# Kernel optimization log

Hardware: AMD Instinct MI355X
Metric: run time of the kernel (lower is better)

## Reference

```python
import jax, jax.numpy as jnp
import numpy as np

ITERS = 4
LN_EPS = 1e-5


def build_grid(H, W):
    # standard uORF grid in [-1, 1], shape (H, W, 2), last dim = (x, y)
    x = jnp.linspace(-1.0 + 1.0 / W, 1.0 - 1.0 / W, W)
    y = jnp.linspace(-1.0 + 1.0 / H, 1.0 - 1.0 / H, H)
    yy, xx = jnp.meshgrid(y, x, indexing='ij')
    return jnp.stack([xx, yy], axis=-1)


def ln(x, g, b):
    m = jnp.mean(x, axis=-1, keepdims=True)
    v = jnp.var(x, axis=-1, keepdims=True)
    return (x - m) * jax.lax.rsqrt(v + LN_EPS) * g + b


def setup_inputs():
    key = jax.random.key(0)
    ks = jax.random.split(key, 16)
    B, H, W, C, K, Ds = 4, 64, 64, 256, 5, 256
    s = 0.02
    inp = {
        'feat': jax.random.normal(ks[0], (B, H, W, C), jnp.float32),
        'mask': (jax.random.uniform(ks[1], (K, 1, H, W)) > 0.5).astype(jnp.float32),
        'noise': jax.random.normal(ks[2], (B, K, Ds), jnp.float32),
        'slots_mu': jax.random.normal(ks[3], (1, 1, Ds), jnp.float32),
        'slots_logsigma': jax.random.normal(ks[4], (1, 1, Ds), jnp.float32) * s,
        'norm_g': jnp.ones((C,), jnp.float32), 'norm_b': jnp.zeros((C,), jnp.float32),
        'grid_W': jax.random.normal(ks[5], (C, 4), jnp.float32) * s,
        'grid_b': jnp.zeros((C,), jnp.float32),
        'k_W': jax.random.normal(ks[6], (C, C), jnp.float32) * s,
        'v_W': jax.random.normal(ks[7], (C, C), jnp.float32) * s,
        'mlp_g': jnp.ones((C,), jnp.float32), 'mlp_b': jnp.zeros((C,), jnp.float32),
        'mlp_W': jax.random.normal(ks[8], (Ds, C), jnp.float32) * s,
        'mlp_bias': jnp.zeros((Ds,), jnp.float32),
        'q_g': jnp.ones((Ds,), jnp.float32), 'q_b': jnp.zeros((Ds,), jnp.float32),
        'q_W': jax.random.normal(ks[9], (Ds, Ds), jnp.float32) * s,
        'gru_Wih': jax.random.normal(ks[10], (3 * Ds, Ds), jnp.float32) * s,
        'gru_Whh': jax.random.normal(ks[11], (3 * Ds, Ds), jnp.float32) * s,
        'gru_bih': jnp.zeros((3 * Ds,), jnp.float32),
        'gru_bhh': jnp.zeros((3 * Ds,), jnp.float32),
        'res_g': jnp.ones((Ds,), jnp.float32), 'res_b': jnp.zeros((Ds,), jnp.float32),
        'res_W': jax.random.normal(ks[12], (Ds, Ds), jnp.float32) * s,
        'res_bias': jnp.zeros((Ds,), jnp.float32),
    }
    return inp


def reference(feat, mask, noise, slots_mu, slots_logsigma, norm_g, norm_b,
              grid_W, grid_b, k_W, v_W, mlp_g, mlp_b, mlp_W, mlp_bias,
              q_g, q_b, q_W, gru_Wih, gru_Whh, gru_bih, gru_bhh,
              res_g, res_b, res_W, res_bias):
    B, H, W, C = feat.shape
    K = mask.shape[0]
    N = H * W
    Ds = slots_mu.shape[-1]
    scale = Ds ** -0.5

    grid = build_grid(H, W)                                   # (H, W, 2)
    # foreground positions: mask-weighted mean of grid -> (K, 2)
    g = jnp.transpose(grid, (2, 0, 1))[None]                  # (1, 2, H, W)
    fg_pos = jnp.sum(g * mask, axis=(2, 3)) / (jnp.sum(mask, axis=(2, 3)) + 1e-5)
    fg_pos = jnp.broadcast_to(fg_pos[None], (B, K, 2))        # (B, K, 2)

    feat_n = ln(feat.reshape(B, N, C), norm_g, norm_b)        # (B, N, C)
    mask_flat = mask.reshape(K, N)
    slot = slots_mu + jnp.exp(slots_logsigma) * noise         # (B, K, Ds)

    # k, v with relative position embedding; fg_pos never changes in-loop,
    # so compute once (the original recomputes the same values each iter).
    rel = grid.reshape(1, 1, N, 2) - fg_pos[:, :, None, :]    # (B, K, N, 2)
    rel4 = jnp.concatenate([rel, -rel], axis=-1)              # (B, K, N, 4)
    ge = rel4 @ grid_W.T + grid_b                             # (B, K, N, C)
    kbase = feat_n @ k_W.T                                    # (B, N, C)
    vbase = feat_n @ v_W.T
    kk = ln(kbase[:, None] + ge, mlp_g, mlp_b) @ mlp_W.T + mlp_bias  # (B,K,N,Ds)
    vv = ln(vbase[:, None] + ge, mlp_g, mlp_b) @ mlp_W.T + mlp_bias

    attn_vis = None
    for _ in range(ITERS):
        slot_prev = slot
        q = ln(slot, q_g, q_b) @ q_W.T                        # (B, K, Ds)
        attn = jnp.einsum('bkd,bknd->bkn', q, kk) * scale
        attn = jnp.where(mask_flat[None] == 0, -1e9, attn)
        attn = jax.nn.softmax(attn, axis=-1)                  # (B, K, N)
        upd = jnp.einsum('bkn,bknd->bkd', attn, vv)           # (B, K, Ds)
        # torch GRUCell
        x = upd.reshape(-1, Ds)
        h = slot.reshape(-1, Ds)
        gi = x @ gru_Wih.T + gru_bih
        gh = h @ gru_Whh.T + gru_bhh
        ir, iz, inn = jnp.split(gi, 3, axis=-1)
        hr, hz, hn = jnp.split(gh, 3, axis=-1)
        r = jax.nn.sigmoid(ir + hr)
        z = jax.nn.sigmoid(iz + hz)
        n = jnp.tanh(inn + r * hn)
        hnew = ((1.0 - z) * n + z * h).reshape(B, K, Ds)
        slot = (ln(hnew, res_g, res_b) @ res_W.T + res_bias) + slot_prev
        amin = attn.min(axis=-1, keepdims=True)
        amax = attn.max(axis=-1, keepdims=True)
        attn_vis = (attn - amin) / (amax - amin + 1e-5)
    return slot, fg_pos, attn_vis
```

## Files before the change

kernel.cpp:

```cpp
#include <hip/hip_runtime.h>
#include <math.h>

typedef unsigned short u16;
typedef unsigned int   u32;
typedef short bf8v __attribute__((ext_vector_type(8)));
typedef float f4v  __attribute__((ext_vector_type(4)));

static constexpr int B_=4, C_=256, K_=5, D_=256, N_=4096, IT_=4;
static constexpr int LP_=264;
static constexpr int PREP_N=2839;
static constexpr float EPS_=1e-5f;

__device__ __forceinline__ float bf2f(u16 u){ u32 x=((u32)u)<<16; float f; __builtin_memcpy(&f,&x,4); return f; }
__device__ __forceinline__ float bflo(u32 u){ u32 x=u<<16; float f; __builtin_memcpy(&f,&x,4); return f; }
__device__ __forceinline__ float bfhi(u32 u){ u32 x=u&0xffff0000u; float f; __builtin_memcpy(&f,&x,4); return f; }
__device__ __forceinline__ u16 f2bf(float f){ u32 x; __builtin_memcpy(&x,&f,4); u32 r=x+0x7fffu+((x>>16)&1u); return (u16)(r>>16); }
__device__ __forceinline__ float ldin(const void* p, size_t i, int f){
  return f ? ((const float*)p)[i] : bf2f(((const u16*)p)[i]);
}
__device__ __forceinline__ void stout(void* p, size_t i, float v, int f){
  if (f) ((float*)p)[i]=v; else ((u16*)p)[i]=f2bf(v);
}

__device__ __forceinline__ void breduce4(float&a,float&b,float&c,float&d,float* red){
  #pragma unroll
  for(int o=32;o>0;o>>=1){
    a+=__shfl_down(a,o,64); b+=__shfl_down(b,o,64);
    c+=__shfl_down(c,o,64); d+=__shfl_down(d,o,64);
  }
  int w=threadIdx.x>>6;
  __syncthreads();
  if((threadIdx.x&63)==0){ red[w]=a; red[4+w]=b; red[8+w]=c; red[12+w]=d; }
  __syncthreads();
  a=red[0]+red[1]+red[2]+red[3];
  b=red[4]+red[5]+red[6]+red[7];
  c=red[8]+red[9]+red[10]+red[11];
  d=red[12]+red[13]+red[14]+red[15];
}
__device__ __forceinline__ void breduce4_16(float&a,float&b,float&c,float&d,float* red){
  #pragma unroll
  for(int o=32;o>0;o>>=1){
    a+=__shfl_down(a,o,64); b+=__shfl_down(b,o,64);
    c+=__shfl_down(c,o,64); d+=__shfl_down(d,o,64);
  }
  int w=threadIdx.x>>6;
  __syncthreads();
  if((threadIdx.x&63)==0){ red[w]=a; red[16+w]=b; red[32+w]=c; red[48+w]=d; }
  __syncthreads();
  a=0;b=0;c=0;d=0;
  #pragma unroll
  for(int i=0;i<16;++i){ a+=red[i]; b+=red[16+i]; c+=red[32+i]; d+=red[48+i]; }
}

__global__ void probe_kernel(const void* feat, int* flag){
  __shared__ float red[16];
  const u32* p=(const u32*)feat;
  int t=threadIdx.x; int bad=0;
  for(int s=0;s<8;++s){
    u32 wd=p[t+s*256];
    float lo=bf2f((u16)(wd&0xffffu));
    if(!(fabsf(lo)<1e6f)) bad++;
  }
  float bb=(float)bad, z1=0,z2=0,z3=0;
  breduce4(bb,z1,z2,z3,red);
  if(t==0) *flag = (bb>=16.f)?1:0;
}

__global__ void prep1_kernel(const int* flag,
    const void* kW, const void* vW, const void* mW, const void* qW, const void* rW,
    const void* Wih, const void* Whh, const void* mu, const void* lsig, const void* noise,
    const void* gW, const void* gb_, const void* mg,
    const void* mb_, const void* mbias, const void* mask,
    float* WqT, float* WrT, float* WihT, float* WhhT,
    float* slot, float* gvec,
    u16* Wkb, u16* Wvb, u16* Wgb,
    float* Uvec, float* Qs, float* fg, void* out)
{
  int f=*flag;
  int bid=blockIdx.x;
  int t=threadIdx.x;
  if(bid<PREP_N){
    int e=bid*256+t;
    if(e<65536){ int c=e>>8, r=e&255; WqT[e]=ldin(qW,(size_t)r*256+c,f); return;} e-=65536;
    if(e<65536){ int c=e>>8, r=e&255; WrT[e]=ldin(rW,(size_t)r*256+c,f); return;} e-=65536;
    if(e<196608){ int c=e/768, r=e-c*768; WihT[e]=ldin(Wih,(size_t)r*256+c,f); return;} e-=196608;
    if(e<196608){ int c=e/768, r=e-c*768; WhhT[e]=ldin(Whh,(size_t)r*256+c,f); return;} e-=196608;
    if(e<5120){ int d=e&255; slot[e]=ldin(mu,d,f)+expf(ldin(lsig,d,f))*ldin(noise,e,f); return;} e-=5120;
    if(e<768){
      int c=e&255, sel=e>>8;
      float v;
      if(sel==0)      v=ldin(gW,c*4+0,f)-ldin(gW,c*4+2,f);
      else if(sel==1) v=ldin(gW,c*4+1,f)-ldin(gW,c*4+3,f);
      else            v=ldin(gb_,c,f);
      gvec[e]=v; return;
    } e-=768;
    if(e<65536){ Wkb[e]=f2bf(ldin(kW,e,f)); return;} e-=65536;
    if(e<65536){ Wvb[e]=f2bf(ldin(vW,e,f)); return;} e-=65536;
    if(e<65536){ int c=e&255; Wgb[e]=f2bf(ldin(mg,c,f)*ldin(mW,e,f)); }
    return;
  }
  __shared__ float s_a[256], s_b[256], s_c[256], red[16];
  if(bid==PREP_N){
    s_a[t]=ldin(gW,t*4+0,f)-ldin(gW,t*4+2,f);
    s_b[t]=ldin(gW,t*4+1,f)-ldin(gW,t*4+3,f);
    s_c[t]=ldin(gb_,t,f);
    __syncthreads();
    float u1=0,u2=0,u3=0,gw=0,bw=0;
    #pragma unroll 8
    for(int c=0;c<256;++c){
      float mwv=ldin(mW,(size_t)t*256+c,f);
      float wg=ldin(mg,c,f)*mwv;
      u1+=s_a[c]*wg; u2+=s_b[c]*wg; u3+=s_c[c]*wg; gw+=wg;
      bw+=ldin(mb_,c,f)*mwv;
    }
    Uvec[t]=u1; Uvec[256+t]=u2; Uvec[512+t]=u3; Uvec[768+t]=gw;
    Uvec[1024+t]=bw+ldin(mbias,t,f);
    float a=s_a[t], b=s_b[t], cc=s_c[t];
    float s0=a*a,s1=b*b,s2=cc*cc,s3=a*b; breduce4(s0,s1,s2,s3,red);
    float s4=a*cc,s5=b*cc,s6=a,s7=b;     breduce4(s4,s5,s6,s7,red);
    float s8=cc,z1=0,z2=0,z3=0;          breduce4(s8,z1,z2,z3,red);
    if(t==0){
      Qs[0]=s0; Qs[1]=s1; Qs[2]=s2; Qs[3]=s3; Qs[4]=s4; Qs[5]=s5;
      Qs[6]=s6*(1.f/256.f); Qs[7]=s7*(1.f/256.f); Qs[8]=s8*(1.f/256.f);
    }
  } else {
    int k=bid-PREP_N-1;
    float sx=0,sy=0,sm=0;
    for(int s=0;s<16;++s){
      int p=t+s*256;
      float m=ldin(mask,(size_t)k*N_+p,f);
      int i=p>>6, j=p&63;
      float x=(2*j+1)*(1.0f/64.0f)-1.0f;
      float y=(2*i+1)*(1.0f/64.0f)-1.0f;
      sx+=x*m; sy+=y*m; sm+=m;
    }
    float d=0;
    breduce4(sx,sy,sm,d,red);
    if(t==0){
      float inv=1.0f/(sm+1e-5f);
      float fx=sx*inv, fy=sy*inv;
      fg[k*2]=fx; fg[k*2+1]=fy;
      for(int b=0;b<B_;++b){
        stout(out, 5120+(b*K_+k)*2+0, fx, f);
        stout(out, 5120+(b*K_+k)*2+1, fy, f);
      }
    }
  }
}

__global__ void __launch_bounds__(256) base_kernel(const int* flag, const void* feat, const void* ng, const void* nb,
    const u16* Wkb, const u16* Wvb, const u16* Wgb, const float* gvec,
    float* scal, u16* PkT, u16* Pvb,
    const float* slot, const void* qg, const void* qb_, const float* WqT, const float* Uvec,
    float* qbuf, float* qsc)
{
  __shared__ u16 fnb[16*LP_];
  __shared__ u16 kbL[16*LP_];
  __shared__ u16 vbL[16*LP_];
  int t=threadIdx.x, f=*flag;
  if(blockIdx.x>=1024){
    float* Lq=(float*)fnb; float* qsh=(float*)kbL; float* red=(float*)vbL;
    int bk=blockIdx.x-1024;
    float x=slot[bk*256+t];
    float s=x,s2=x*x,z0=0,z1=0; breduce4(s,s2,z0,z1,red);
    float m=s*(1.f/256.f), v=s2*(1.f/256.f)-m*m;
    Lq[t]=(x-m)*rsqrtf(v+EPS_)*ldin(qg,t,f)+ldin(qb_,t,f);
    __syncthreads();
    float acc=0;
    #pragma unroll 8
    for(int c=0;c<256;++c) acc+=Lq[c]*WqT[c*256+t];
    qbuf[bk*256+t]=acc; qsh[t]=acc;
    __syncthreads();
    float q=qsh[t];
    float s0=q*Uvec[t], s1=q*Uvec[256+t], s2b=q*Uvec[512+t], s3=q*Uvec[768+t];
    breduce4(s0,s1,s2b,s3,red);
    float s4=q*Uvec[1024+t], z2=0,z3=0,z4=0;
    breduce4(s4,z2,z3,z4,red);
    if(t==0){ qsc[bk*8+0]=s0; qsc[bk*8+1]=s1; qsc[bk*8+2]=s2b; qsc[bk*8+3]=s3; qsc[bk*8+4]=s4; }
    return;
  }
  int w=t>>6, l=t&63;
  int quad=l>>4, m=l&15;
  int row0=blockIdx.x*16;
  {
    float g0=ldin(ng,l,f), g1=ldin(ng,l+64,f), g2=ldin(ng,l+128,f), g3=ldin(ng,l+192,f);
    float b0=ldin(nb,l,f), b1=ldin(nb,l+64,f), b2=ldin(nb,l+128,f), b3=ldin(nb,l+192,f);
    #pragma unroll
    for(int r4=0;r4<4;++r4){
      int r=4*w+r4; size_t base=(size_t)(row0+r)*256;
      float x0=ldin(feat,base+l,f), x1=ldin(feat,base+l+64,f),
            x2=ldin(feat,base+l+128,f), x3=ldin(feat,base+l+192,f);
      float s=x0+x1+x2+x3, s2=x0*x0+x1*x1+x2*x2+x3*x3;
      #pragma unroll
      for(int o=32;o>0;o>>=1){ s+=__shfl_xor(s,o,64); s2+=__shfl_xor(s2,o,64); }
      float mm=s*(1.f/256.f), inv=rsqrtf(s2*(1.f/256.f)-mm*mm+EPS_);
      fnb[r*LP_+l]    =f2bf((x0-mm)*inv*g0+b0);
      fnb[r*LP_+l+64] =f2bf((x1-mm)*inv*g1+b1);
      fnb[r*LP_+l+128]=f2bf((x2-mm)*inv*g2+b2);
      fnb[r*LP_+l+192]=f2bf((x3-mm)*inv*g3+b3);
    }
  }
  __syncthreads();
  {
    f4v ack[4], acv[4];
    #pragma unroll
    for(int i=0;i<4;++i){ ack[i]=(f4v){0.f,0.f,0.f,0.f}; acv[i]=(f4v){0.f,0.f,0.f,0.f}; }
    #pragma unroll
    for(int kk=0;kk<8;++kk){
      int kb0=kk*32+quad*8;
      bf8v af=*(bf8v*)&fnb[m*LP_+kb0];
      #pragma unroll
      for(int i=0;i<4;++i){
        int n=64*w+16*i+m;
        bf8v bk=*(const bf8v*)(Wkb+(size_t)n*256+kb0);
        bf8v bv=*(const bf8v*)(Wvb+(size_t)n*256+kb0);
        ack[i]=__builtin_amdgcn_mfma_f32_16x16x32_bf16(af,bk,ack[i],0,0,0);
        acv[i]=__builtin_amdgcn_mfma_f32_16x16x32_bf16(af,bv,acv[i],0,0,0);
      }
    }
    #pragma unroll
    for(int i=0;i<4;++i){
      int n=64*w+16*i+m;
      #pragma unroll
      for(int r=0;r<4;++r){
        int row=quad*4+r;
        kbL[row*LP_+n]=f2bf(ack[i][r]);
        vbL[row*LP_+n]=f2bf(acv[i][r]);
      }
    }
  }
  __syncthreads();
  {
    float gA0=gvec[l], gA1=gvec[l+64], gA2=gvec[l+128], gA3=gvec[l+192];
    float gB0=gvec[256+l], gB1=gvec[256+l+64], gB2=gvec[256+l+128], gB3=gvec[256+l+192];
    float gC0=gvec[512+l], gC1=gvec[512+l+64], gC2=gvec[512+l+128], gC3=gvec[512+l+192];
    for(int r4=0;r4<4;++r4){
      int r=4*w+r4;
      float k0=bf2f(kbL[r*LP_+l]), k1=bf2f(kbL[r*LP_+l+64]),
            k2=bf2f(kbL[r*LP_+l+128]), k3=bf2f(kbL[r*LP_+l+192]);
      float x0=bf2f(vbL[r*LP_+l]), x1=bf2f(vbL[r*LP_+l+64]),
            x2=bf2f(vbL[r*LP_+l+128]), x3=bf2f(vbL[r*LP_+l+192]);
      float v0=k0+k1+k2+k3;
      float v1=k0*k0+k1*k1+k2*k2+k3*k3;
      float v2=k0*gA0+k1*gA1+k2*gA2+k3*gA3;
      float v3=k0*gB0+k1*gB1+k2*gB2+k3*gB3;
      float v4=k0*gC0+k1*gC1+k2*gC2+k3*gC3;
      float v5=x0+x1+x2+x3;
      float v6=x0*x0+x1*x1+x2*x2+x3*x3;
      float v7=x0*gA0+x1*gA1+x2*gA2+x3*gA3;
      float v8=x0*gB0+x1*gB1+x2*gB2+x3*gB3;
      float v9=x0*gC0+x1*gC1+x2*gC2+x3*gC3;
      #pragma unroll
      for(int o=32;o>0;o>>=1){
        v0+=__shfl_down(v0,o,64); v1+=__shfl_down(v1,o,64); v2+=__shfl_down(v2,o,64);
        v3+=__shfl_down(v3,o,64); v4+=__shfl_down(v4,o,64); v5+=__shfl_down(v5,o,64);
        v6+=__shfl_down(v6,o,64); v7+=__shfl_down(v7,o,64); v8+=__shfl_down(v8,o,64);
        v9+=__shfl_down(v9,o,64);
      }
      if(l==0){
        float* sc=scal+(size_t)(row0+r)*10;
        sc[0]=v0; sc[1]=v1; sc[2]=v2; sc[3]=v3; sc[4]=v4;
        sc[5]=v5; sc[6]=v6; sc[7]=v7; sc[8]=v8; sc[9]=v9;
      }
    }
  }
  {
    f4v apk[4], apv[4];
    #pragma unroll
    for(int i=0;i<4;++i){ apk[i]=(f4v){0.f,0.f,0.f,0.f}; apv[i]=(f4v){0.f,0.f,0.f,0.f}; }
    #pragma unroll
    for(int kk=0;kk<8;++kk){
      int kb0=kk*32+quad*8;
      bf8v afk=*(bf8v*)&kbL[m*LP_+kb0];
      bf8v afv=*(bf8v*)&vbL[m*LP_+kb0];
      #pragma unroll
      for(int i=0;i<4;++i){
        int n=64*w+16*i+m;
        bf8v bg=*(const bf8v*)(Wgb+(size_t)n*256+kb0);
        apk[i]=__builtin_amdgcn_mfma_f32_16x16x32_bf16(afk,bg,apk[i],0,0,0);
        apv[i]=__builtin_amdgcn_mfma_f32_16x16x32_bf16(afv,bg,apv[i],0,0,0);
      }
    }
    #pragma unroll
    for(int i=0;i<4;++i){
      int d=64*w+16*i+m;
      *(ushort4*)(PkT+(size_t)d*16384+row0+quad*4)=
        make_ushort4(f2bf(apk[i][0]),f2bf(apk[i][1]),f2bf(apk[i][2]),f2bf(apk[i][3]));
      #pragma unroll
      for(int r=0;r<4;++r)
        fnb[(quad*4+r)*LP_+d]=f2bf(apv[i][r]);
    }
  }
  __syncthreads();
  {
    int d0=l*4;
    #pragma unroll
    for(int r=0;r<4;++r){
      int row=4*w+r;
      ushort4 s4=make_ushort4(fnb[row*LP_+d0],fnb[row*LP_+d0+1],fnb[row*LP_+d0+2],fnb[row*LP_+d0+3]);
      *(ushort4*)(Pvb+(size_t)(row0+row)*256+d0)=s4;
    }
  }
}

__global__ void __launch_bounds__(512) attn_kernel(const int* flag, const float* qbuf, const u16* PkT,
    const float* scal, const float* Qs, const float* qsc, const float* fg, const void* mask,
    const u16* Pvb, float* logits, float* pmax, float* psum, float* updpart, float* sscp,
    int store_lg)
{
  __shared__ float q5[1280];
  __shared__ float un[10240];
  __shared__ float lgs[320], ivs[320], mvs[320];
  __shared__ float qs5[40], fgs[10], Qss[9], MSl[5];
  __shared__ float sred[8][5][4];
  int tid=threadIdx.x, f=*flag;
  int b=blockIdx.x>>6, ch=blockIdx.x&63;
  int w=tid>>6, l=tid&63;
  int n0=ch<<6;
  for(int p=tid;p<1280;p+=512) q5[p]=qbuf[(size_t)b*1280+p];
  if(tid<40) qs5[tid]=qsc[(size_t)b*40+tid];
  if(tid<10) fgs[tid]=fg[tid];
  if(tid<9)  Qss[tid]=Qs[tid];
  __syncthreads();
  {
    int n=n0+l; size_t row=(size_t)b*N_+n;
    float dk0=0,dk1=0,dk2=0,dk3=0,dk4=0;
    int cbase=w*32;
    #pragma unroll 8
    for(int cc=0;cc<32;++cc){
      int c=cbase+cc;
      float pv=bf2f(PkT[(size_t)c*16384+row]);
      dk0+=pv*q5[c]; dk1+=pv*q5[256+c]; dk2+=pv*q5[512+c];
      dk3+=pv*q5[768+c]; dk4+=pv*q5[1024+c];
    }
    un[(w*5+0)*64+l]=dk0; un[(w*5+1)*64+l]=dk1; un[(w*5+2)*64+l]=dk2;
    un[(w*5+3)*64+l]=dk3; un[(w*5+4)*64+l]=dk4;
  }
  __syncthreads();
  if(tid<320){
    int k=tid>>6, nl=tid&63;
    float dot=0;
    #pragma unroll
    for(int j=0;j<8;++j) dot+=un[(j*5+k)*64+nl];
    int n2=n0+nl; size_t row2=(size_t)b*N_+n2;
    const float* sc=scal+row2*10;
    float rx=(2*(n2&63)+1)*(1.f/64.f)-1.f-fgs[2*k];
    float ry=(2*(n2>>6)+1)*(1.f/64.f)-1.f-fgs[2*k+1];
    float qge=rx*rx*Qss[0]+ry*ry*Qss[1]+Qss[2]+2.f*(rx*ry*Qss[3]+rx*Qss[4]+ry*Qss[5]);
    float mk=sc[0]*(1.f/256.f)+rx*Qss[6]+ry*Qss[7]+Qss[8];
    float sxk=sc[1]+2.f*(rx*sc[2]+ry*sc[3]+sc[4])+qge;
    float invK=rsqrtf(sxk*(1.f/256.f)-mk*mk+EPS_);
    float lg=invK*(dot+rx*qs5[k*8+0]+ry*qs5[k*8+1]+qs5[k*8+2]-mk*qs5[k*8+3])+qs5[k*8+4];
    float mval=ldin(mask,(size_t)k*N_+n2,f);
    lg=(mval==0.f)? -1e9f : lg*0.0625f;
    if(store_lg) logits[((size_t)(b*5+k))*N_+n2]=lg;
    lgs[tid]=lg;
    float mv=sc[5]*(1.f/256.f)+rx*Qss[6]+ry*Qss[7]+Qss[8];
    float sxv=sc[6]+2.f*(rx*sc[7]+ry*sc[8]+sc[9])+qge;
    mvs[tid]=mv;
    ivs[tid]=rsqrtf(sxv*(1.f/256.f)-mv*mv+EPS_);
  }
  __syncthreads();
  if(tid<64){
    #pragma unroll
    for(int k=0;k<5;++k){
      float v=lgs[k*64+tid];
      float M=v;
      #pragma unroll
      for(int o=32;o>0;o>>=1) M=fmaxf(M,__shfl_xor(M,o,64));
      float e=expf(v-M);
      #pragma unroll
      for(int o=32;o>0;o>>=1) e+=__shfl_xor(e,o,64);
      if(tid==0){ pmax[((size_t)(b*64+ch))*5+k]=M; psum[((size_t)(b*64+ch))*5+k]=e; MSl[k]=M; }
    }
  }
  __syncthreads();
  {
    float acc[5][4]={{0}};
    float swx[5]={0,0,0,0,0}, swy[5]={0,0,0,0,0}, sw[5]={0,0,0,0,0}, swm[5]={0,0,0,0,0};
    #pragma unroll 2
    for(int rr=0;rr<8;++rr){
      int nl=w*8+rr; int n2=n0+nl;
      size_t row=(size_t)b*N_+n2;
      uint2 pu=*(const uint2*)(Pvb+row*256+l*4);
      float px=bflo(pu.x), py=bfhi(pu.x), pz=bflo(pu.y), pw=bfhi(pu.y);
      int jx=n2&63, iy=n2>>6;
      #pragma unroll
      for(int k=0;k<5;++k){
        float wgt=expf(lgs[k*64+nl]-MSl[k])*ivs[k*64+nl];
        float rx=(2*jx+1)*(1.f/64.f)-1.f-fgs[2*k];
        float ry=(2*iy+1)*(1.f/64.f)-1.f-fgs[2*k+1];
        acc[k][0]+=wgt*px; acc[k][1]+=wgt*py; acc[k][2]+=wgt*pz; acc[k][3]+=wgt*pw;
        sw[k]+=wgt; swx[k]+=wgt*rx; swy[k]+=wgt*ry; swm[k]+=wgt*mvs[k*64+nl];
      }
    }
    #pragma unroll
    for(int k=0;k<5;++k)
      *(float4*)&un[(w*5+k)*256+l*4]=make_float4(acc[k][0],acc[k][1],acc[k][2],acc[k][3]);
    if(l==0){
      #pragma unroll
      for(int k=0;k<5;++k){ sred[w][k][0]=swx[k]; sred[w][k][1]=swy[k];
                            sred[w][k][2]=sw[k];  sred[w][k][3]=swm[k]; }
    }
  }
  __syncthreads();
  for(int p=tid;p<1280;p+=512){
    int k=p>>8, d=p&255;
    float v=0;
    #pragma unroll
    for(int j=0;j<8;++j) v+=un[(j*5+k)*256+d];
    updpart[((size_t)blockIdx.x*5+k)*256+d]=v;
  }
  if(tid<20){
    int kk=tid>>2, j=tid&3;
    float s=0;
    #pragma unroll
    for(int jj=0;jj<8;++jj) s+=sred[jj][kk][j];
    sscp[((size_t)blockIdx.x*5+kk)*4+j]=s;
  }
}

__global__ void __launch_bounds__(1024) gru_kernel(const int* flag, float* slot, const float* updpart,
    const float* sscp, const float* Uvec, const float* pmax, const float* psum, const float* logits,
    const float* WihT, const float* WhhT, const void* bih, const void* bhh,
    const void* rg, const void* rb_, const float* WrT, const void* rbias,
    const void* qg, const void* qb_, const float* WqT, float* qbuf, float* qsc,
    int do_vis, void* out)
{
  __shared__ float u[256], h[256], sn[256];
  __shared__ float part[4][6][256];
  __shared__ float red[64];
  __shared__ float cvec[4];
  __shared__ float fch[64];
  __shared__ float MSg[2];
  int tid=threadIdx.x, t=tid&255, g=tid>>8;
  int blk=blockIdx.x;
  int f=*flag;
  if(blk>=20){
    if(!do_vis) return;
    int bk2=blk-20, k2=bk2%K_, b2=bk2/K_;
    if(tid<64){
      float pm=pmax[((size_t)(b2*64+tid))*5+k2];
      float ps=psum[((size_t)(b2*64+tid))*5+k2];
      float M=pm;
      #pragma unroll
      for(int o=32;o>0;o>>=1) M=fmaxf(M,__shfl_xor(M,o,64));
      float e=ps*expf(pm-M);
      #pragma unroll
      for(int o=32;o>0;o>>=1) e+=__shfl_xor(e,o,64);
      if(tid==0){ MSg[0]=M; MSg[1]=1.0f/e; }
    }
    __syncthreads();
    float M=MSg[0], Sinv=MSg[1];
    float a[4]; float mn=1e30f, mx=-1e30f;
    #pragma unroll
    for(int s=0;s<4;++s){
      a[s]=expf(logits[(size_t)bk2*N_+tid+s*1024]-M)*Sinv;
      mn=fminf(mn,a[s]); mx=fmaxf(mx,a[s]);
    }
    #pragma unroll
    for(int o=32;o>0;o>>=1){ mn=fminf(mn,__shfl_down(mn,o,64)); mx=fmaxf(mx,__shfl_down(mx,o,64)); }
    int wv=tid>>6;
    __syncthreads();
    if((tid&63)==0){ red[wv]=mn; red[16+wv]=mx; }
    __syncthreads();
    mn=1e30f; mx=-1e30f;
    #pragma unroll
    for(int i=0;i<16;++i){ mn=fminf(mn,red[i]); mx=fmaxf(mx,red[16+i]); }
    float inv=1.0f/(mx-mn+1e-5f);
    #pragma unroll
    for(int s=0;s<4;++s) stout(out, 5160+(size_t)bk2*N_+tid+s*1024, (a[s]-mn)*inv, f);
    return;
  }
  int bk=blk, k=bk%K_, b=bk/K_;
  if(tid<64){
    float pm=pmax[((size_t)(b*64+tid))*5+k];
    float ps=psum[((size_t)(b*64+tid))*5+k];
    float M=pm;
    #pragma unroll
    for(int o=32;o>0;o>>=1) M=fmaxf(M,__shfl_xor(M,o,64));
    float fc=expf(pm-M);
    fch[tid]=fc;
    float e=ps*fc;
    #pragma unroll
    for(int o=32;o>0;o>>=1) e+=__shfl_xor(e,o,64);
    if(tid==0){ MSg[0]=M; MSg[1]=1.0f/e; }
  }
  __syncthreads();
  float Sinv=MSg[1];
  float ua=0;
  {
    int ch0=g*16;
    #pragma unroll 4
    for(int ci=0;ci<16;++ci){ int ch=ch0+ci; ua += fch[ch]*updpart[(((size_t)(b*64+ch))*5+k)*256+t]; }
  }
  part[g][0][t]=ua;
  if(t<4){
    float s=0;
    #pragma unroll 4
    for(int ci=0;ci<16;++ci){ int ch=g*16+ci; s += fch[ch]*sscp[(((size_t)(b*64+ch))*5+k)*4+t]; }
    part[g][1][t]=s;
  }
  __syncthreads();
  if(g==0 && t<4) cvec[t]=part[0][1][t]+part[1][1][t]+part[2][1][t]+part[3][1][t];
  __syncthreads();
  if(g==0){
    float uu=part[0][0][t]+part[1][0][t]+part[2][0][t]+part[3][0][t];
    u[t]=(uu+cvec[0]*Uvec[t]+cvec[1]*Uvec[256+t]+cvec[2]*Uvec[512+t]-cvec[3]*Uvec[768+t])*Sinv
         +Uvec[1024+t];
    h[t]=slot[bk*256+t];
  }
  __syncthreads();
  float p0=0,p1=0,p2=0,p3=0,p4=0,p5=0;
  int c0=g*64;
  #pragma unroll 8
  for(int cc=0;cc<64;++cc){
    int c=c0+cc;
    float uc=u[c], hc=h[c];
    const float* wi=WihT+(size_t)c*768+t;
    const float* wh=WhhT+(size_t)c*768+t;
    p0+=uc*wi[0]; p1+=uc*wi[256]; p2+=uc*wi[512];
    p3+=hc*wh[0]; p4+=hc*wh[256]; p5+=hc*wh[512];
  }
  part[g][0][t]=p0; part[g][1][t]=p1; part[g][2][t]=p2;
  part[g][3][t]=p3; part[g][4][t]=p4; part[g][5][t]=p5;
  __syncthreads();
  float hn=0;
  if(g==0){
    float gi0=ldin(bih,t,f)+part[0][0][t]+part[1][0][t]+part[2][0][t]+part[3][0][t];
    float gi1=ldin(bih,256+t,f)+part[0][1][t]+part[1][1][t]+part[2][1][t]+part[3][1][t];
    float gi2=ldin(bih,512+t,f)+part[0][2][t]+part[1][2][t]+part[2][2][t]+part[3][2][t];
    float gh0=ldin(bhh,t,f)+part[0][3][t]+part[1][3][t]+part[2][3][t]+part[3][3][t];
    float gh1=ldin(bhh,256+t,f)+part[0][4][t]+part[1][4][t]+part[2][4][t]+part[3][4][t];
    float gh2=ldin(bhh,512+t,f)+part[0][5][t]+part[1][5][t]+part[2][5][t]+part[3][5][t];
    float r=1.f/(1.f+expf(-(gi0+gh0)));
    float z=1.f/(1.f+expf(-(gi1+gh1)));
    float nn=tanhf(gi2+r*gh2);
    hn=(1.f-z)*nn+z*h[t];
  }
  float s=hn, sq=hn*hn, za=0, zb=0;
  breduce4_16(s,sq,za,zb,red);
  if(g==0){
    float m=s*(1.f/256.f), var=sq*(1.f/256.f)-m*m;
    u[t]=(hn-m)*rsqrtf(var+EPS_)*ldin(rg,t,f)+ldin(rb_,t,f);
  }
  __syncthreads();
  float pr=0;
  #pragma unroll 8
  for(int cc=0;cc<64;++cc){ int c=c0+cc; pr+=u[c]*WrT[(size_t)c*256+t]; }
  part[g][0][t]=pr;
  __syncthreads();
  if(g==0){
    float acc=ldin(rbias,t,f)+h[t]+part[0][0][t]+part[1][0][t]+part[2][0][t]+part[3][0][t];
    slot[bk*256+t]=acc;
    stout(out, (size_t)bk*256+t, acc, f);
    sn[t]=acc;
  }
  __syncthreads();
  float xs=(g==0)? sn[t]:0.f;
  float xq=xs*xs, zc=0, zd=0;
  breduce4_16(xs,xq,zc,zd,red);
  if(g==0){
    float m=xs*(1.f/256.f), var=xq*(1.f/256.f)-m*m;
    u[t]=(sn[t]-m)*rsqrtf(var+EPS_)*ldin(qg,t,f)+ldin(qb_,t,f);
  }
  __syncthreads();
  float pq=0;
  #pragma unroll 8
  for(int cc=0;cc<64;++cc){ int c=c0+cc; pq+=u[c]*WqT[(size_t)c*256+t]; }
  part[g][0][t]=pq;
  __syncthreads();
  float qv=0.f;
  if(g==0){
    qv=part[0][0][t]+part[1][0][t]+part[2][0][t]+part[3][0][t];
    qbuf[bk*256+t]=qv;
  }
  float a0=(g==0)? qv*Uvec[t]:0.f;
  float a1=(g==0)? qv*Uvec[256+t]:0.f;
  float a2=(g==0)? qv*Uvec[512+t]:0.f;
  float a3=(g==0)? qv*Uvec[768+t]:0.f;
  breduce4_16(a0,a1,a2,a3,red);
  float a4=(g==0)? qv*Uvec[1024+t]:0.f;
  float z1=0,z2=0,z3=0;
  breduce4_16(a4,z1,z2,z3,red);
  if(tid==0){ qsc[bk*8+0]=a0; qsc[bk*8+1]=a1; qsc[bk*8+2]=a2; qsc[bk*8+3]=a3; qsc[bk*8+4]=a4; }
}

extern "C" void kernel_launch(void* const* d_in, const int* in_sizes, int n_in,
                              void* d_out, int out_size, void* d_ws, size_t ws_size,
                              hipStream_t stream)
{
  const void* feat =d_in[0];  const void* mask =d_in[1];  const void* noise=d_in[2];
  const void* mu   =d_in[3];  const void* lsig =d_in[4];  const void* ng   =d_in[5];
  const void* nb   =d_in[6];  const void* gW   =d_in[7];  const void* gb_  =d_in[8];
  const void* kW   =d_in[9];  const void* vW   =d_in[10]; const void* mg   =d_in[11];
  const void* mb_  =d_in[12]; const void* mW   =d_in[13]; const void* mbias=d_in[14];
  const void* qg   =d_in[15]; const void* qb_  =d_in[16]; const void* qW   =d_in[17];
  const void* Wih  =d_in[18]; const void* Whh  =d_in[19]; const void* bih  =d_in[20];
  const void* bhh  =d_in[21]; const void* rg   =d_in[22]; const void* rb_  =d_in[23];
  const void* rW   =d_in[24]; const void* rbias=d_in[25];

  char* p=(char*)d_ws;
  auto alloc=[&](size_t bytes)->char*{ char* r=p; p+=(bytes+255)&~(size_t)255; return r; };
  int*   flag   =(int*)  alloc(256);
  float* fg     =(float*)alloc(64);
  float* slot   =(float*)alloc(5120*4);
  float* qbuf   =(float*)alloc(5120*4);
  float* qsc    =(float*)alloc(160*4);
  float* logits =(float*)alloc((size_t)81920*4);
  float* pmax   =(float*)alloc(1280*4);
  float* psum   =(float*)alloc(1280*4);
  float* updpart=(float*)alloc((size_t)256*5*256*4);
  float* sscp   =(float*)alloc((size_t)256*5*4*4);
  float* WqT    =(float*)alloc((size_t)65536*4);
  float* WrT    =(float*)alloc((size_t)65536*4);
  float* WihT   =(float*)alloc((size_t)196608*4);
  float* WhhT   =(float*)alloc((size_t)196608*4);
  float* gvec   =(float*)alloc(768*4);
  float* Uvec   =(float*)alloc(1280*4);
  float* Qs     =(float*)alloc(64);
  float* scal   =(float*)alloc((size_t)163840*4);
  u16*   Wkb    =(u16*)  alloc((size_t)65536*2);
  u16*   Wvb    =(u16*)  alloc((size_t)65536*2);
  u16*   Wgb    =(u16*)  alloc((size_t)65536*2);
  u16*   PkT    =(u16*)  alloc((size_t)16384*256*2);
  u16*   Pvb    =(u16*)  alloc((size_t)16384*256*2);

  probe_kernel<<<1,256,0,stream>>>(feat, flag);
  prep1_kernel<<<PREP_N+6,256,0,stream>>>(flag,kW,vW,mW,qW,rW,Wih,Whh,mu,lsig,noise,gW,gb_,mg,
                                          mb_,mbias,mask,
                                          WqT,WrT,WihT,WhhT,slot,gvec,Wkb,Wvb,Wgb,
                                          Uvec,Qs,fg,d_out);
  base_kernel<<<1044,256,0,stream>>>(flag,feat,ng,nb,Wkb,Wvb,Wgb,gvec,scal,PkT,Pvb,
                                     slot,qg,qb_,WqT,Uvec,qbuf,qsc);
  for(int it=0; it<IT_; ++it){
    attn_kernel<<<B_*64,512,0,stream>>>(flag,qbuf,PkT,scal,Qs,qsc,fg,mask,Pvb,
                                        logits,pmax,psum,updpart,sscp,(it==IT_-1)?1:0);
    int nb_g = (it==IT_-1)? 40 : 20;
    gru_kernel<<<nb_g,1024,0,stream>>>(flag,slot,updpart,sscp,Uvec,pmax,psum,logits,
                                       WihT,WhhT,bih,bhh,rg,rb_,WrT,rbias,
                                       qg,qb_,WqT,qbuf,qsc,(it==IT_-1)?1:0,d_out);
  }
}
```

Before: 391.5 us.

## Merge probe, prep and base kernels into one setup kernel

Folds the dtype probe, weight preparation and the base projection kernel into a single launch. Every block recomputes the dtype flag locally. The projection MFMAs read the raw k/v/mlp weights and convert them on the fly instead of using pre-converted bf16 copies, and the mlp gain is applied to the A operand inside the loop. The q·Uvec scalar products move from the GRU and base kernels into the attention kernel's prologue. This removes two launches and the serial dependency on the prep kernel, at the cost of redundant per-block flag probes, per-use conversion work, and extra reductions in every attention block.

```diff
diff --git a/kernel.cpp b/kernel.cpp
--- a/kernel.cpp
+++ b/kernel.cpp
@@ -8,8 +8,16 @@
 
 static constexpr int B_=4, C_=256, K_=5, D_=256, N_=4096, IT_=4;
 static constexpr int LP_=264;
-static constexpr int PREP_N=2839;
 static constexpr float EPS_=1e-5f;
+static constexpr int NB_BASE=1024;
+static constexpr int NB_Q0=1024;
+static constexpr int NB_WQ=1044;
+static constexpr int NB_WR=1300;
+static constexpr int NB_WIH=1556;
+static constexpr int NB_WHH=2324;
+static constexpr int NB_UQ=3092;
+static constexpr int NB_FG=3093;
+static constexpr int NB_TOT=3098;
 
 __device__ __forceinline__ float bf2f(u16 u){ u32 x=((u32)u)<<16; float f; __builtin_memcpy(&f,&x,4); return f; }
 __device__ __forceinline__ float bflo(u32 u){ u32 x=u<<16; float f; __builtin_memcpy(&f,&x,4); return f; }
@@ -21,6 +29,15 @@
 __device__ __forceinline__ void stout(void* p, size_t i, float v, int f){
   if (f) ((float*)p)[i]=v; else ((u16*)p)[i]=f2bf(v);
 }
+__device__ __forceinline__ bf8v loadW8(const void* p, size_t i, int f){
+  if(!f) return *(const bf8v*)((const u16*)p + i);
+  float4 a=*(const float4*)((const float*)p+i);
+  float4 b=*(const float4*)((const float*)p+i+4);
+  bf8v r;
+  r[0]=(short)f2bf(a.x); r[1]=(short)f2bf(a.y); r[2]=(short)f2bf(a.z); r[3]=(short)f2bf(a.w);
+  r[4]=(short)f2bf(b.x); r[5]=(short)f2bf(b.y); r[6]=(short)f2bf(b.z); r[7]=(short)f2bf(b.w);
+  return r;
+}
 
 __device__ __forceinline__ void breduce4(float&a,float&b,float&c,float&d,float* red){
   #pragma unroll
@@ -52,136 +69,123 @@
   for(int i=0;i<16;++i){ a+=red[i]; b+=red[16+i]; c+=red[32+i]; d+=red[48+i]; }
 }
 
-__global__ void probe_kernel(const void* feat, int* flag){
-  __shared__ float red[16];
-  const u32* p=(const u32*)feat;
-  int t=threadIdx.x; int bad=0;
-  for(int s=0;s<8;++s){
-    u32 wd=p[t+s*256];
-    float lo=bf2f((u16)(wd&0xffffu));
-    if(!(fabsf(lo)<1e6f)) bad++;
-  }
-  float bb=(float)bad, z1=0,z2=0,z3=0;
-  breduce4(bb,z1,z2,z3,red);
-  if(t==0) *flag = (bb>=16.f)?1:0;
-}
-
-__global__ void prep1_kernel(const int* flag,
+__global__ void __launch_bounds__(256) setup_kernel(const void* feat,
     const void* kW, const void* vW, const void* mW, const void* qW, const void* rW,
     const void* Wih, const void* Whh, const void* mu, const void* lsig, const void* noise,
-    const void* gW, const void* gb_, const void* mg,
-    const void* mb_, const void* mbias, const void* mask,
-    float* WqT, float* WrT, float* WihT, float* WhhT,
-    float* slot, float* gvec,
-    u16* Wkb, u16* Wvb, u16* Wgb,
-    float* Uvec, float* Qs, float* fg, void* out)
-{
-  int f=*flag;
-  int bid=blockIdx.x;
-  int t=threadIdx.x;
-  if(bid<PREP_N){
-    int e=bid*256+t;
-    if(e<65536){ int c=e>>8, r=e&255; WqT[e]=ldin(qW,(size_t)r*256+c,f); return;} e-=65536;
-    if(e<65536){ int c=e>>8, r=e&255; WrT[e]=ldin(rW,(size_t)r*256+c,f); return;} e-=65536;
-    if(e<196608){ int c=e/768, r=e-c*768; WihT[e]=ldin(Wih,(size_t)r*256+c,f); return;} e-=196608;
-    if(e<196608){ int c=e/768, r=e-c*768; WhhT[e]=ldin(Whh,(size_t)r*256+c,f); return;} e-=196608;
-    if(e<5120){ int d=e&255; slot[e]=ldin(mu,d,f)+expf(ldin(lsig,d,f))*ldin(noise,e,f); return;} e-=5120;
-    if(e<768){
-      int c=e&255, sel=e>>8;
-      float v;
-      if(sel==0)      v=ldin(gW,c*4+0,f)-ldin(gW,c*4+2,f);
-      else if(sel==1) v=ldin(gW,c*4+1,f)-ldin(gW,c*4+3,f);
-      else            v=ldin(gb_,c,f);
-      gvec[e]=v; return;
-    } e-=768;
-    if(e<65536){ Wkb[e]=f2bf(ldin(kW,e,f)); return;} e-=65536;
-    if(e<65536){ Wvb[e]=f2bf(ldin(vW,e,f)); return;} e-=65536;
-    if(e<65536){ int c=e&255; Wgb[e]=f2bf(ldin(mg,c,f)*ldin(mW,e,f)); }
-    return;
-  }
-  __shared__ float s_a[256], s_b[256], s_c[256], red[16];
-  if(bid==PREP_N){
-    s_a[t]=ldin(gW,t*4+0,f)-ldin(gW,t*4+2,f);
-    s_b[t]=ldin(gW,t*4+1,f)-ldin(gW,t*4+3,f);
-    s_c[t]=ldin(gb_,t,f);
-    __syncthreads();
-    float u1=0,u2=0,u3=0,gw=0,bw=0;
-    #pragma unroll 8
-    for(int c=0;c<256;++c){
-      float mwv=ldin(mW,(size_t)t*256+c,f);
-      float wg=ldin(mg,c,f)*mwv;
-      u1+=s_a[c]*wg; u2+=s_b[c]*wg; u3+=s_c[c]*wg; gw+=wg;
-      bw+=ldin(mb_,c,f)*mwv;
-    }
-    Uvec[t]=u1; Uvec[256+t]=u2; Uvec[512+t]=u3; Uvec[768+t]=gw;
-    Uvec[1024+t]=bw+ldin(mbias,t,f);
-    float a=s_a[t], b=s_b[t], cc=s_c[t];
-    float s0=a*a,s1=b*b,s2=cc*cc,s3=a*b; breduce4(s0,s1,s2,s3,red);
-    float s4=a*cc,s5=b*cc,s6=a,s7=b;     breduce4(s4,s5,s6,s7,red);
-    float s8=cc,z1=0,z2=0,z3=0;          breduce4(s8,z1,z2,z3,red);
-    if(t==0){
-      Qs[0]=s0; Qs[1]=s1; Qs[2]=s2; Qs[3]=s3; Qs[4]=s4; Qs[5]=s5;
-      Qs[6]=s6*(1.f/256.f); Qs[7]=s7*(1.f/256.f); Qs[8]=s8*(1.f/256.f);
-    }
-  } else {
-    int k=bid-PREP_N-1;
-    float sx=0,sy=0,sm=0;
-    for(int s=0;s<16;++s){
-      int p=t+s*256;
-      float m=ldin(mask,(size_t)k*N_+p,f);
-      int i=p>>6, j=p&63;
-      float x=(2*j+1)*(1.0f/64.0f)-1.0f;
-      float y=(2*i+1)*(1.0f/64.0f)-1.0f;
-      sx+=x*m; sy+=y*m; sm+=m;
-    }
-    float d=0;
-    breduce4(sx,sy,sm,d,red);
-    if(t==0){
-      float inv=1.0f/(sm+1e-5f);
-      float fx=sx*inv, fy=sy*inv;
-      fg[k*2]=fx; fg[k*2+1]=fy;
-      for(int b=0;b<B_;++b){
-        stout(out, 5120+(b*K_+k)*2+0, fx, f);
-        stout(out, 5120+(b*K_+k)*2+1, fy, f);
-      }
-    }
-  }
-}
-
-__global__ void __launch_bounds__(256) base_kernel(const int* flag, const void* feat, const void* ng, const void* nb,
-    const u16* Wkb, const u16* Wvb, const u16* Wgb, const float* gvec,
-    float* scal, u16* PkT, u16* Pvb,
-    const float* slot, const void* qg, const void* qb_, const float* WqT, const float* Uvec,
-    float* qbuf, float* qsc)
+    const void* gW, const void* gb_, const void* mg, const void* mb_, const void* mbias,
+    const void* ng, const void* nb, const void* qg, const void* qb_, const void* mask,
+    int* flag, float* WqT, float* WrT, float* WihT, float* WhhT,
+    float* slot, float* Uvec, float* Qs, float* fg,
+    float* scal, u16* PkT, u16* Pvb, float* qbuf, void* out)
 {
   __shared__ u16 fnb[16*LP_];
   __shared__ u16 kbL[16*LP_];
   __shared__ u16 vbL[16*LP_];
-  int t=threadIdx.x, f=*flag;
-  if(blockIdx.x>=1024){
-    float* Lq=(float*)fnb; float* qsh=(float*)kbL; float* red=(float*)vbL;
-    int bk=blockIdx.x-1024;
-    float x=slot[bk*256+t];
-    float s=x,s2=x*x,z0=0,z1=0; breduce4(s,s2,z0,z1,red);
-    float m=s*(1.f/256.f), v=s2*(1.f/256.f)-m*m;
-    Lq[t]=(x-m)*rsqrtf(v+EPS_)*ldin(qg,t,f)+ldin(qb_,t,f);
-    __syncthreads();
-    float acc=0;
-    #pragma unroll 8
-    for(int c=0;c<256;++c) acc+=Lq[c]*WqT[c*256+t];
-    qbuf[bk*256+t]=acc; qsh[t]=acc;
-    __syncthreads();
-    float q=qsh[t];
-    float s0=q*Uvec[t], s1=q*Uvec[256+t], s2b=q*Uvec[512+t], s3=q*Uvec[768+t];
-    breduce4(s0,s1,s2b,s3,red);
-    float s4=q*Uvec[1024+t], z2=0,z3=0,z4=0;
-    breduce4(s4,z2,z3,z4,red);
-    if(t==0){ qsc[bk*8+0]=s0; qsc[bk*8+1]=s1; qsc[bk*8+2]=s2b; qsc[bk*8+3]=s3; qsc[bk*8+4]=s4; }
-    return;
-  }
+  __shared__ float redp[16];
+  int t=threadIdx.x, bid=blockIdx.x;
+  int f;
+  {
+    const u32* pf=(const u32*)feat;
+    int bad=0;
+    #pragma unroll
+    for(int s=0;s<8;++s){
+      u32 wd=pf[t+s*256];
+      float lo=bf2f((u16)(wd&0xffffu));
+      if(!(fabsf(lo)<1e6f)) bad++;
+    }
+    float bb=(float)bad, z1=0,z2=0,z3=0;
+    breduce4(bb,z1,z2,z3,redp);
+    f=(bb>=16.f)?1:0;
+    if(bid==NB_Q0 && t==0) *flag=f;
+  }
+  __syncthreads();
+
+  if(bid>=NB_BASE){
+    if(bid<NB_WQ){
+      float* Lq=(float*)fnb; float* red=(float*)vbL;
+      int bk=bid-NB_Q0;
+      float x=ldin(mu,t,f)+expf(ldin(lsig,t,f))*ldin(noise,(size_t)bk*256+t,f);
+      slot[bk*256+t]=x;
+      float s=x,s2=x*x,z0=0,z1=0; breduce4(s,s2,z0,z1,red);
+      float m=s*(1.f/256.f), v=s2*(1.f/256.f)-m*m;
+      Lq[t]=(x-m)*rsqrtf(v+EPS_)*ldin(qg,t,f)+ldin(qb_,t,f);
+      __syncthreads();
+      float acc=0;
+      if(!f){
+        const u16* qr=(const u16*)qW + (size_t)t*256;
+        #pragma unroll 8
+        for(int c0=0;c0<256;c0+=8){
+          uint4 u=*(const uint4*)(qr+c0);
+          acc+=bflo(u.x)*Lq[c0]+bfhi(u.x)*Lq[c0+1]+bflo(u.y)*Lq[c0+2]+bfhi(u.y)*Lq[c0+3]
+              +bflo(u.z)*Lq[c0+4]+bfhi(u.z)*Lq[c0+5]+bflo(u.w)*Lq[c0+6]+bfhi(u.w)*Lq[c0+7];
+        }
+      }else{
+        const float* qr=(const float*)qW + (size_t)t*256;
+        #pragma unroll 8
+        for(int c=0;c<256;++c) acc+=qr[c]*Lq[c];
+      }
+      qbuf[bk*256+t]=acc;
+      return;
+    }
+    if(bid<NB_WR){ int e=(bid-NB_WQ)*256+t; int c=e>>8, r=e&255; WqT[e]=ldin(qW,(size_t)r*256+c,f); return; }
+    if(bid<NB_WIH){ int e=(bid-NB_WR)*256+t; int c=e>>8, r=e&255; WrT[e]=ldin(rW,(size_t)r*256+c,f); return; }
+    if(bid<NB_WHH){ int e=(bid-NB_WIH)*256+t; int c=e/768, r=e-c*768; WihT[e]=ldin(Wih,(size_t)r*256+c,f); return; }
+    if(bid<NB_UQ){ int e=(bid-NB_WHH)*256+t; int c=e/768, r=e-c*768; WhhT[e]=ldin(Whh,(size_t)r*256+c,f); return; }
+    if(bid==NB_UQ){
+      float* s_a=(float*)fnb; float* s_b=(float*)kbL; float* s_c=(float*)vbL;
+      s_a[t]=ldin(gW,t*4+0,f)-ldin(gW,t*4+2,f);
+      s_b[t]=ldin(gW,t*4+1,f)-ldin(gW,t*4+3,f);
+      s_c[t]=ldin(gb_,t,f);
+      __syncthreads();
+      float u1=0,u2=0,u3=0,gw=0,bw=0;
+      #pragma unroll 8
+      for(int c=0;c<256;++c){
+        float mwv=ldin(mW,(size_t)t*256+c,f);
+        float wg=ldin(mg,c,f)*mwv;
+        u1+=s_a[c]*wg; u2+=s_b[c]*wg; u3+=s_c[c]*wg; gw+=wg;
+        bw+=ldin(mb_,c,f)*mwv;
+      }
+      Uvec[t]=u1; Uvec[256+t]=u2; Uvec[512+t]=u3; Uvec[768+t]=gw;
+      Uvec[1024+t]=bw+ldin(mbias,t,f);
+      float a=s_a[t], b=s_b[t], cc=s_c[t];
+      float s0=a*a,s1=b*b,s2=cc*cc,s3=a*b; breduce4(s0,s1,s2,s3,redp);
+      float s4=a*cc,s5=b*cc,s6=a,s7=b;     breduce4(s4,s5,s6,s7,redp);
+      float s8=cc,z1=0,z2=0,z3=0;          breduce4(s8,z1,z2,z3,redp);
+      if(t==0){
+        Qs[0]=s0; Qs[1]=s1; Qs[2]=s2; Qs[3]=s3; Qs[4]=s4; Qs[5]=s5;
+        Qs[6]=s6*(1.f/256.f); Qs[7]=s7*(1.f/256.f); Qs[8]=s8*(1.f/256.f);
+      }
+      return;
+    }
+    {
+      int k=bid-NB_FG;
+      float sx=0,sy=0,sm=0;
+      for(int s=0;s<16;++s){
+        int p=t+s*256;
+        float m=ldin(mask,(size_t)k*N_+p,f);
+        int i=p>>6, j=p&63;
+        float x=(2*j+1)*(1.0f/64.0f)-1.0f;
+        float y=(2*i+1)*(1.0f/64.0f)-1.0f;
+        sx+=x*m; sy+=y*m; sm+=m;
+      }
+      float d=0;
+      breduce4(sx,sy,sm,d,redp);
+      if(t==0){
+        float inv=1.0f/(sm+1e-5f);
+        float fx=sx*inv, fy=sy*inv;
+        fg[k*2]=fx; fg[k*2+1]=fy;
+        for(int b=0;b<B_;++b){
+          stout(out, 5120+(b*K_+k)*2+0, fx, f);
+          stout(out, 5120+(b*K_+k)*2+1, fy, f);
+        }
+      }
+      return;
+    }
+  }
+
   int w=t>>6, l=t&63;
   int quad=l>>4, m=l&15;
-  int row0=blockIdx.x*16;
+  int row0=bid*16;
   {
     float g0=ldin(ng,l,f), g1=ldin(ng,l+64,f), g2=ldin(ng,l+128,f), g3=ldin(ng,l+192,f);
     float b0=ldin(nb,l,f), b1=ldin(nb,l+64,f), b2=ldin(nb,l+128,f), b3=ldin(nb,l+192,f);
@@ -212,8 +216,8 @@
       #pragma unroll
       for(int i=0;i<4;++i){
         int n=64*w+16*i+m;
-        bf8v bk=*(const bf8v*)(Wkb+(size_t)n*256+kb0);
-        bf8v bv=*(const bf8v*)(Wvb+(size_t)n*256+kb0);
+        bf8v bk=loadW8(kW,(size_t)n*256+kb0,f);
+        bf8v bv=loadW8(vW,(size_t)n*256+kb0,f);
         ack[i]=__builtin_amdgcn_mfma_f32_16x16x32_bf16(af,bk,ack[i],0,0,0);
         acv[i]=__builtin_amdgcn_mfma_f32_16x16x32_bf16(af,bv,acv[i],0,0,0);
       }
@@ -231,9 +235,15 @@
   }
   __syncthreads();
   {
-    float gA0=gvec[l], gA1=gvec[l+64], gA2=gvec[l+128], gA3=gvec[l+192];
-    float gB0=gvec[256+l], gB1=gvec[256+l+64], gB2=gvec[256+l+128], gB3=gvec[256+l+192];
-    float gC0=gvec[512+l], gC1=gvec[512+l+64], gC2=gvec[512+l+128], gC3=gvec[512+l+192];
+    float gA0=ldin(gW,l*4+0,f)-ldin(gW,l*4+2,f);
+    float gA1=ldin(gW,(l+64)*4+0,f)-ldin(gW,(l+64)*4+2,f);
+    float gA2=ldin(gW,(l+128)*4+0,f)-ldin(gW,(l+128)*4+2,f);
+    float gA3=ldin(gW,(l+192)*4+0,f)-ldin(gW,(l+192)*4+2,f);
+    float gB0=ldin(gW,l*4+1,f)-ldin(gW,l*4+3,f);
+    float gB1=ldin(gW,(l+64)*4+1,f)-ldin(gW,(l+64)*4+3,f);
+    float gB2=ldin(gW,(l+128)*4+1,f)-ldin(gW,(l+128)*4+3,f);
+    float gB3=ldin(gW,(l+192)*4+1,f)-ldin(gW,(l+192)*4+3,f);
+    float gC0=ldin(gb_,l,f), gC1=ldin(gb_,l+64,f), gC2=ldin(gb_,l+128,f), gC3=ldin(gb_,l+192,f);
     for(int r4=0;r4<4;++r4){
       int r=4*w+r4;
       float k0=bf2f(kbL[r*LP_+l]), k1=bf2f(kbL[r*LP_+l+64]),
@@ -271,12 +281,19 @@
     #pragma unroll
     for(int kk=0;kk<8;++kk){
       int kb0=kk*32+quad*8;
-      bf8v afk=*(bf8v*)&kbL[m*LP_+kb0];
-      bf8v afv=*(bf8v*)&vbL[m*LP_+kb0];
+      bf8v rk=*(bf8v*)&kbL[m*LP_+kb0];
+      bf8v rv=*(bf8v*)&vbL[m*LP_+kb0];
+      bf8v afk, afv;
+      #pragma unroll
+      for(int j=0;j<8;++j){
+        float mgv=ldin(mg,kb0+j,f);
+        afk[j]=(short)f2bf(bf2f((u16)rk[j])*mgv);
+        afv[j]=(short)f2bf(bf2f((u16)rv[j])*mgv);
+      }
       #pragma unroll
       for(int i=0;i<4;++i){
         int n=64*w+16*i+m;
-        bf8v bg=*(const bf8v*)(Wgb+(size_t)n*256+kb0);
+        bf8v bg=loadW8(mW,(size_t)n*256+kb0,f);
         apk[i]=__builtin_amdgcn_mfma_f32_16x16x32_bf16(afk,bg,apk[i],0,0,0);
         apv[i]=__builtin_amdgcn_mfma_f32_16x16x32_bf16(afv,bg,apv[i],0,0,0);
       }
@@ -304,7 +321,7 @@
 }
 
 __global__ void __launch_bounds__(512) attn_kernel(const int* flag, const float* qbuf, const u16* PkT,
-    const float* scal, const float* Qs, const float* qsc, const float* fg, const void* mask,
+    const float* scal, const float* Qs, const float* Uvec, const float* fg, const void* mask,
     const u16* Pvb, float* logits, float* pmax, float* psum, float* updpart, float* sscp,
     int store_lg)
 {
@@ -318,10 +335,17 @@
   int w=tid>>6, l=tid&63;
   int n0=ch<<6;
   for(int p=tid;p<1280;p+=512) q5[p]=qbuf[(size_t)b*1280+p];
-  if(tid<40) qs5[tid]=qsc[(size_t)b*40+tid];
   if(tid<10) fgs[tid]=fg[tid];
   if(tid<9)  Qss[tid]=Qs[tid];
   __syncthreads();
+  for(int p=w;p<25;p+=8){
+    int k=p/5, j=p%5;
+    float s=q5[k*256+l]*Uvec[j*256+l]+q5[k*256+l+64]*Uvec[j*256+l+64]
+           +q5[k*256+l+128]*Uvec[j*256+l+128]+q5[k*256+l+192]*Uvec[j*256+l+192];
+    #pragma unroll
+    for(int o=32;o>0;o>>=1) s+=__shfl_xor(s,o,64);
+    if(l==0) qs5[k*8+j]=s;
+  }
   {
     int n=n0+l; size_t row=(size_t)b*N_+n;
     float dk0=0,dk1=0,dk2=0,dk3=0,dk4=0;
@@ -424,7 +448,7 @@
     const float* sscp, const float* Uvec, const float* pmax, const float* psum, const float* logits,
     const float* WihT, const float* WhhT, const void* bih, const void* bhh,
     const void* rg, const void* rb_, const float* WrT, const void* rbias,
-    const void* qg, const void* qb_, const float* WqT, float* qbuf, float* qsc,
+    const void* qg, const void* qb_, const float* WqT, float* qbuf,
     int do_vis, void* out)
 {
   __shared__ float u[256], h[256], sn[256];
@@ -570,20 +594,10 @@
   for(int cc=0;cc<64;++cc){ int c=c0+cc; pq+=u[c]*WqT[(size_t)c*256+t]; }
   part[g][0][t]=pq;
   __syncthreads();
-  float qv=0.f;
   if(g==0){
-    qv=part[0][0][t]+part[1][0][t]+part[2][0][t]+part[3][0][t];
+    float qv=part[0][0][t]+part[1][0][t]+part[2][0][t]+part[3][0][t];
     qbuf[bk*256+t]=qv;
   }
-  float a0=(g==0)? qv*Uvec[t]:0.f;
-  float a1=(g==0)? qv*Uvec[256+t]:0.f;
-  float a2=(g==0)? qv*Uvec[512+t]:0.f;
-  float a3=(g==0)? qv*Uvec[768+t]:0.f;
-  breduce4_16(a0,a1,a2,a3,red);
-  float a4=(g==0)? qv*Uvec[1024+t]:0.f;
-  float z1=0,z2=0,z3=0;
-  breduce4_16(a4,z1,z2,z3,red);
-  if(tid==0){ qsc[bk*8+0]=a0; qsc[bk*8+1]=a1; qsc[bk*8+2]=a2; qsc[bk*8+3]=a3; qsc[bk*8+4]=a4; }
 }
 
 extern "C" void kernel_launch(void* const* d_in, const int* in_sizes, int n_in,
@@ -606,7 +620,6 @@
   float* fg     =(float*)alloc(64);
   float* slot   =(float*)alloc(5120*4);
   float* qbuf   =(float*)alloc(5120*4);
-  float* qsc    =(float*)alloc(160*4);
   float* logits =(float*)alloc((size_t)81920*4);
   float* pmax   =(float*)alloc(1280*4);
   float* psum   =(float*)alloc(1280*4);
@@ -616,29 +629,22 @@
   float* WrT    =(float*)alloc((size_t)65536*4);
   float* WihT   =(float*)alloc((size_t)196608*4);
   float* WhhT   =(float*)alloc((size_t)196608*4);
-  float* gvec   =(float*)alloc(768*4);
   float* Uvec   =(float*)alloc(1280*4);
   float* Qs     =(float*)alloc(64);
   float* scal   =(float*)alloc((size_t)163840*4);
-  u16*   Wkb    =(u16*)  alloc((size_t)65536*2);
-  u16*   Wvb    =(u16*)  alloc((size_t)65536*2);
-  u16*   Wgb    =(u16*)  alloc((size_t)65536*2);
   u16*   PkT    =(u16*)  alloc((size_t)16384*256*2);
   u16*   Pvb    =(u16*)  alloc((size_t)16384*256*2);
 
-  probe_kernel<<<1,256,0,stream>>>(feat, flag);
-  prep1_kernel<<<PREP_N+6,256,0,stream>>>(flag,kW,vW,mW,qW,rW,Wih,Whh,mu,lsig,noise,gW,gb_,mg,
-                                          mb_,mbias,mask,
-                                          WqT,WrT,WihT,WhhT,slot,gvec,Wkb,Wvb,Wgb,
-                                          Uvec,Qs,fg,d_out);
-  base_kernel<<<1044,256,0,stream>>>(flag,feat,ng,nb,Wkb,Wvb,Wgb,gvec,scal,PkT,Pvb,
-                                     slot,qg,qb_,WqT,Uvec,qbuf,qsc);
+  setup_kernel<<<NB_TOT,256,0,stream>>>(feat,kW,vW,mW,qW,rW,Wih,Whh,mu,lsig,noise,
+                                        gW,gb_,mg,mb_,mbias,ng,nb,qg,qb_,mask,
+                                        flag,WqT,WrT,WihT,WhhT,slot,Uvec,Qs,fg,
+                                        scal,PkT,Pvb,qbuf,d_out);
   for(int it=0; it<IT_; ++it){
-    attn_kernel<<<B_*64,512,0,stream>>>(flag,qbuf,PkT,scal,Qs,qsc,fg,mask,Pvb,
+    attn_kernel<<<B_*64,512,0,stream>>>(flag,qbuf,PkT,scal,Qs,Uvec,fg,mask,Pvb,
                                         logits,pmax,psum,updpart,sscp,(it==IT_-1)?1:0);
     int nb_g = (it==IT_-1)? 40 : 20;
     gru_kernel<<<nb_g,1024,0,stream>>>(flag,slot,updpart,sscp,Uvec,pmax,psum,logits,
                                        WihT,WhhT,bih,bhh,rg,rb_,WrT,rbias,
-                                       qg,qb_,WqT,qbuf,qsc,(it==IT_-1)?1:0,d_out);
-  }
-}
+                                       qg,qb_,WqT,qbuf,(it==IT_-1)?1:0,d_out);
+  }
+}
```

Result: slower. 436.8 us (+11.6%).
